# Kernel tuning notes

Hardware: AMD Instinct MI355X
Metric: run time of the kernel (lower is better)

Reference implementation:

```python
import jax, jax.numpy as jnp
import numpy as np

N_ITEM_TYPE = 18
N_ITEM_FEAT = 11
N_TYPE_HIDDEN = 32
N_ITEM_HIDDEN = 128
BS, NA, NI = 32, 128, 128


def setup_inputs() -> dict:
    key = jax.random.key(0)
    k1, k2, k3, k4 = jax.random.split(key, 4)
    item_type = jax.random.randint(k1, (BS, NA, NI), 0, N_ITEM_TYPE, dtype=jnp.int64)
    item = jax.random.normal(k2, (BS, NA, NI, N_ITEM_FEAT), dtype=jnp.float32)
    emb = jax.random.normal(k3, (N_ITEM_TYPE, N_TYPE_HIDDEN), dtype=jnp.float32)
    W = jax.random.normal(k4, (N_TYPE_HIDDEN + N_ITEM_FEAT, N_ITEM_HIDDEN), dtype=jnp.float32) * 0.1
    b = jnp.zeros((N_ITEM_HIDDEN,), dtype=jnp.float32)
    return {"item_type": item_type, "item": item, "emb": emb, "W": W, "b": b}


def reference(item_type, item, emb, W, b):
    # embedding gather: [bs, na, ni, 32]
    h_type = emb[item_type]
    # concat features: [bs, na, ni, 43]
    h = jnp.concatenate([h_type, item], axis=-1)
    # Linear + ReLU: [bs, na, ni, n_item_hidden]
    h = jax.nn.relu(jnp.einsum("bnif,fh->bnih", h, W) + b)
    # max-pool over item axis: [bs, na, n_item_hidden]
    return jnp.max(h, axis=2)
```

## Files before the change

kernel.cpp:

```cpp
#include <hip/hip_runtime.h>
#include <hip/hip_bf16.h>
#include <stdint.h>


#define NITEM  128
#define NFEAT  11
#define NTH    32
#define NH     128
#define KREAL  43
#define KSTEPS 3
#define BNPB   4
#define SLABDW (NITEM * NFEAT)

typedef __attribute__((ext_vector_type(8)))  _Float16 half8;
typedef __attribute__((ext_vector_type(2)))  __fp16   fp16x2;
typedef __attribute__((ext_vector_type(16))) float    f32x16;

union H8 { half8 h8; fp16x2 h2[4]; };

__global__ __launch_bounds__(64) void prep_b(const float* __restrict__ W,
                                             _Float16* __restrict__ Bpre) {
    const int frag = blockIdx.x;
    const int kk   = frag >> 2;
    const int n    = frag & 3;
    const int lane = threadIdx.x;
    const int col  = n * 32 + (lane & 31);
    const int k0   = kk * 16 + (lane >> 5) * 8;
    half8 pk;
    #pragma unroll
    for (int q = 0; q < 8; ++q) {
        const int k = k0 + q;
        pk[q] = (_Float16)((k < KREAL) ? W[k * NH + col] : 0.0f);
    }
    ((half8*)Bpre)[frag * 64 + lane] = pk;
}

__global__ __launch_bounds__(256, 2) void item_encoder(
    const int*      __restrict__ item_type,
    const float*    __restrict__ item,
    const float*    __restrict__ emb,
    const _Float16* __restrict__ Bpre,
    const float*    __restrict__ bias,
    float*          __restrict__ out)
{
    __shared__ float slab[BNPB * SLABDW];
    __shared__ int   typs[BNPB * NITEM];
    __shared__ float partial[BNPB][4][NH];

    const int t    = threadIdx.x;
    const int lane = t & 63;
    const int w    = t >> 6;
    const int l31  = lane & 31;
    const int lhi  = lane >> 5;
    const int bn0  = blockIdx.x * BNPB;

    half8 bf[KSTEPS][4];
    #pragma unroll
    for (int kk = 0; kk < KSTEPS; ++kk)
        #pragma unroll
        for (int n = 0; n < 4; ++n)
            bf[kk][n] = ((const half8*)Bpre)[(kk * 4 + n) * 64 + lane];

    {
        const float4* gsl = (const float4*)(item + (size_t)bn0 * SLABDW);
        float4*       lsl = (float4*)slab;
        #pragma unroll
        for (int j = 0; j < 5; ++j) lsl[t + 256 * j] = gsl[t + 256 * j];
        if (t < 128) lsl[1280 + t] = gsl[1280 + t];
        if (t < 128)
            ((int4*)typs)[t] = ((const int4*)(item_type + (size_t)bn0 * NITEM))[t];
    }
    __syncthreads();

    const int r = w * 32 + l31;
    float bias4[4];
    #pragma unroll
    for (int n = 0; n < 4; ++n) bias4[n] = bias[n * 32 + l31];

    #pragma unroll 1
    for (int b = 0; b < BNPB; ++b) {
        const int    ty = typs[b * NITEM + r];
        const float* eb = emb + ty * NTH;

        const float4 e0 = *(const float4*)(eb + lhi * 8);
        const float4 e1 = *(const float4*)(eb + lhi * 8 + 4);
        const float4 e2 = *(const float4*)(eb + 16 + lhi * 8);
        const float4 e3 = *(const float4*)(eb + 16 + lhi * 8 + 4);

        H8 a0, a1, a2;
        a0.h2[0] = __builtin_amdgcn_cvt_pkrtz(e0.x, e0.y);
        a0.h2[1] = __builtin_amdgcn_cvt_pkrtz(e0.z, e0.w);
        a0.h2[2] = __builtin_amdgcn_cvt_pkrtz(e1.x, e1.y);
        a0.h2[3] = __builtin_amdgcn_cvt_pkrtz(e1.z, e1.w);
        a1.h2[0] = __builtin_amdgcn_cvt_pkrtz(e2.x, e2.y);
        a1.h2[1] = __builtin_amdgcn_cvt_pkrtz(e2.z, e2.w);
        a1.h2[2] = __builtin_amdgcn_cvt_pkrtz(e3.x, e3.y);
        a1.h2[3] = __builtin_amdgcn_cvt_pkrtz(e3.z, e3.w);

        const float* sp = slab + b * SLABDW + r * NFEAT;
        float fv[8];
        #pragma unroll
        for (int q = 0; q < 8; ++q) {
            const int f  = lhi * 8 + q;
            const bool ok = (f < NFEAT);
            const float x = sp[ok ? f : 0];
            fv[q] = ok ? x : 0.0f;
        }
        a2.h2[0] = __builtin_amdgcn_cvt_pkrtz(fv[0], fv[1]);
        a2.h2[1] = __builtin_amdgcn_cvt_pkrtz(fv[2], fv[3]);
        a2.h2[2] = __builtin_amdgcn_cvt_pkrtz(fv[4], fv[5]);
        a2.h2[3] = __builtin_amdgcn_cvt_pkrtz(fv[6], fv[7]);

        f32x16 acc[4];
        #pragma unroll
        for (int n = 0; n < 4; ++n)
            #pragma unroll
            for (int rr = 0; rr < 16; ++rr) acc[n][rr] = 0.0f;

        #pragma unroll
        for (int n = 0; n < 4; ++n) acc[n] = __builtin_amdgcn_mfma_f32_32x32x16_f16(a0.h8, bf[0][n], acc[n], 0, 0, 0);
        #pragma unroll
        for (int n = 0; n < 4; ++n) acc[n] = __builtin_amdgcn_mfma_f32_32x32x16_f16(a1.h8, bf[1][n], acc[n], 0, 0, 0);
        #pragma unroll
        for (int n = 0; n < 4; ++n) acc[n] = __builtin_amdgcn_mfma_f32_32x32x16_f16(a2.h8, bf[2][n], acc[n], 0, 0, 0);

        #pragma unroll
        for (int n = 0; n < 4; ++n) {
            float m = acc[n][0];
            #pragma unroll
            for (int rr = 1; rr < 16; ++rr) m = fmaxf(m, acc[n][rr]);
            m = fmaxf(m, __shfl_xor(m, 32));
            m = fmaxf(m + bias4[n], 0.0f);
            if (lane < 32) partial[b][w][n * 32 + l31] = m;
        }
    }

    __syncthreads();

    #pragma unroll
    for (int jj = 0; jj < 2; ++jj) {
        const int idx = t + 256 * jj;
        const int b   = idx >> 7;
        const int col = idx & 127;
        float m = fmaxf(fmaxf(partial[b][0][col], partial[b][1][col]),
                        fmaxf(partial[b][2][col], partial[b][3][col]));
        out[(size_t)(bn0 + b) * NH + col] = m;
    }
}

extern "C" void kernel_launch(void* const* d_in, const int* in_sizes, int n_in,
                              void* d_out, int out_size, void* d_ws, size_t ws_size,
                              hipStream_t stream) {
    const int*   item_type = (const int*)  d_in[0];
    const float* item      = (const float*)d_in[1];
    const float* emb       = (const float*)d_in[2];
    const float* W         = (const float*)d_in[3];
    const float* bias      = (const float*)d_in[4];
    float*       out       = (float*)d_out;
    _Float16*    Bpre      = (_Float16*)d_ws;

    prep_b<<<12, 64, 0, stream>>>(W, Bpre);
    item_encoder<<<(32 * 128) / BNPB, 256, 0, stream>>>(item_type, item, emb, Bpre, bias, out);
}
```

Measured before the change: 91.07 us.

## Assign one (batch,agent) row per wave and drop cross-wave partial reduction

New measurement: 89.49 us. No clear change (-1.7%).

```diff
diff --git a/kernel.cpp b/kernel.cpp
--- a/kernel.cpp
+++ b/kernel.cpp
@@ -1,6 +1,7 @@
 #include <hip/hip_runtime.h>
 #include <hip/hip_bf16.h>
 #include <stdint.h>
+#include <float.h>
 
 
 #define NITEM  128
@@ -44,8 +45,6 @@
     float*          __restrict__ out)
 {
     __shared__ float slab[BNPB * SLABDW];
-    __shared__ int   typs[BNPB * NITEM];
-    __shared__ float partial[BNPB][4][NH];
 
     const int t    = threadIdx.x;
     const int lane = t & 63;
@@ -53,6 +52,22 @@
     const int l31  = lane & 31;
     const int lhi  = lane >> 5;
     const int bn0  = blockIdx.x * BNPB;
+    const int bn   = bn0 + w;
+
+    int ty[4];
+    {
+        const int* tb = item_type + (size_t)bn * NITEM + l31;
+        #pragma unroll
+        for (int rb = 0; rb < 4; ++rb) ty[rb] = tb[rb * 32];
+    }
+
+    {
+        const float4* gsl = (const float4*)(item + (size_t)bn0 * SLABDW);
+        float4*       lsl = (float4*)slab;
+        #pragma unroll
+        for (int j = 0; j < 5; ++j) lsl[t + 256 * j] = gsl[t + 256 * j];
+        if (t < 128) lsl[1280 + t] = gsl[1280 + t];
+    }
 
     half8 bf[KSTEPS][4];
     #pragma unroll
@@ -61,51 +76,47 @@
         for (int n = 0; n < 4; ++n)
             bf[kk][n] = ((const half8*)Bpre)[(kk * 4 + n) * 64 + lane];
 
-    {
-        const float4* gsl = (const float4*)(item + (size_t)bn0 * SLABDW);
-        float4*       lsl = (float4*)slab;
-        #pragma unroll
-        for (int j = 0; j < 5; ++j) lsl[t + 256 * j] = gsl[t + 256 * j];
-        if (t < 128) lsl[1280 + t] = gsl[1280 + t];
-        if (t < 128)
-            ((int4*)typs)[t] = ((const int4*)(item_type + (size_t)bn0 * NITEM))[t];
+    float4 E[4][4];
+    #pragma unroll
+    for (int rb = 0; rb < 4; ++rb) {
+        const float* eb = emb + ty[rb] * NTH + lhi * 8;
+        E[rb][0] = *(const float4*)(eb);
+        E[rb][1] = *(const float4*)(eb + 4);
+        E[rb][2] = *(const float4*)(eb + 16);
+        E[rb][3] = *(const float4*)(eb + 20);
     }
-    __syncthreads();
 
-    const int r = w * 32 + l31;
     float bias4[4];
     #pragma unroll
     for (int n = 0; n < 4; ++n) bias4[n] = bias[n * 32 + l31];
 
-    #pragma unroll 1
-    for (int b = 0; b < BNPB; ++b) {
-        const int    ty = typs[b * NITEM + r];
-        const float* eb = emb + ty * NTH;
+    __syncthreads();
 
-        const float4 e0 = *(const float4*)(eb + lhi * 8);
-        const float4 e1 = *(const float4*)(eb + lhi * 8 + 4);
-        const float4 e2 = *(const float4*)(eb + 16 + lhi * 8);
-        const float4 e3 = *(const float4*)(eb + 16 + lhi * 8 + 4);
+    float vm[4] = { -FLT_MAX, -FLT_MAX, -FLT_MAX, -FLT_MAX };
 
-        H8 a0, a1, a2;
-        a0.h2[0] = __builtin_amdgcn_cvt_pkrtz(e0.x, e0.y);
-        a0.h2[1] = __builtin_amdgcn_cvt_pkrtz(e0.z, e0.w);
-        a0.h2[2] = __builtin_amdgcn_cvt_pkrtz(e1.x, e1.y);
-        a0.h2[3] = __builtin_amdgcn_cvt_pkrtz(e1.z, e1.w);
-        a1.h2[0] = __builtin_amdgcn_cvt_pkrtz(e2.x, e2.y);
-        a1.h2[1] = __builtin_amdgcn_cvt_pkrtz(e2.z, e2.w);
-        a1.h2[2] = __builtin_amdgcn_cvt_pkrtz(e3.x, e3.y);
-        a1.h2[3] = __builtin_amdgcn_cvt_pkrtz(e3.z, e3.w);
+    #pragma unroll
+    for (int rb = 0; rb < 4; ++rb) {
+        const int r = rb * 32 + l31;
+        const float* sp = slab + w * SLABDW + r * NFEAT;
 
-        const float* sp = slab + b * SLABDW + r * NFEAT;
         float fv[8];
         #pragma unroll
         for (int q = 0; q < 8; ++q) {
-            const int f  = lhi * 8 + q;
+            const int  f  = lhi * 8 + q;
             const bool ok = (f < NFEAT);
             const float x = sp[ok ? f : 0];
             fv[q] = ok ? x : 0.0f;
         }
+
+        H8 a0, a1, a2;
+        a0.h2[0] = __builtin_amdgcn_cvt_pkrtz(E[rb][0].x, E[rb][0].y);
+        a0.h2[1] = __builtin_amdgcn_cvt_pkrtz(E[rb][0].z, E[rb][0].w);
+        a0.h2[2] = __builtin_amdgcn_cvt_pkrtz(E[rb][1].x, E[rb][1].y);
+        a0.h2[3] = __builtin_amdgcn_cvt_pkrtz(E[rb][1].z, E[rb][1].w);
+        a1.h2[0] = __builtin_amdgcn_cvt_pkrtz(E[rb][2].x, E[rb][2].y);
+        a1.h2[1] = __builtin_amdgcn_cvt_pkrtz(E[rb][2].z, E[rb][2].w);
+        a1.h2[2] = __builtin_amdgcn_cvt_pkrtz(E[rb][3].x, E[rb][3].y);
+        a1.h2[3] = __builtin_amdgcn_cvt_pkrtz(E[rb][3].z, E[rb][3].w);
         a2.h2[0] = __builtin_amdgcn_cvt_pkrtz(fv[0], fv[1]);
         a2.h2[1] = __builtin_amdgcn_cvt_pkrtz(fv[2], fv[3]);
         a2.h2[2] = __builtin_amdgcn_cvt_pkrtz(fv[4], fv[5]);
@@ -130,21 +141,14 @@
             #pragma unroll
             for (int rr = 1; rr < 16; ++rr) m = fmaxf(m, acc[n][rr]);
             m = fmaxf(m, __shfl_xor(m, 32));
-            m = fmaxf(m + bias4[n], 0.0f);
-            if (lane < 32) partial[b][w][n * 32 + l31] = m;
+            vm[n] = fmaxf(vm[n], m);
         }
     }
 
-    __syncthreads();
-
-    #pragma unroll
-    for (int jj = 0; jj < 2; ++jj) {
-        const int idx = t + 256 * jj;
-        const int b   = idx >> 7;
-        const int col = idx & 127;
-        float m = fmaxf(fmaxf(partial[b][0][col], partial[b][1][col]),
-                        fmaxf(partial[b][2][col], partial[b][3][col]));
-        out[(size_t)(bn0 + b) * NH + col] = m;
+    if (lane < 32) {
+        #pragma unroll
+        for (int n = 0; n < 4; ++n)
+            out[(size_t)bn * NH + n * 32 + l31] = fmaxf(vm[n] + bias4[n], 0.0f);
     }
 }
 
```
